# Kernel tuning notes

Measured on AMD Instinct MI355X. Metric: run time of the kernel, lower is better.

## Reference

```python
import jax, jax.numpy as jnp
import numpy as np

EMBED_DIM = 1024
NUM_HEADS = 16
D_K = EMBED_DIM // NUM_HEADS
SEQ = 4096
BATCH = 1


def setup_inputs() -> dict:
    key = jax.random.key(0)
    ks = jax.random.split(key, 9)
    s = 1.0 / np.sqrt(EMBED_DIM)
    return {
        "x": jax.random.normal(ks[0], (BATCH, SEQ, EMBED_DIM), dtype=jnp.float32),
        "Wq": jax.random.normal(ks[1], (EMBED_DIM, EMBED_DIM), dtype=jnp.float32) * s,
        "bq": jax.random.normal(ks[2], (EMBED_DIM,), dtype=jnp.float32) * 0.02,
        "Wk": jax.random.normal(ks[3], (EMBED_DIM, EMBED_DIM), dtype=jnp.float32) * s,
        "bk": jax.random.normal(ks[4], (EMBED_DIM,), dtype=jnp.float32) * 0.02,
        "Wv": jax.random.normal(ks[5], (EMBED_DIM, EMBED_DIM), dtype=jnp.float32) * s,
        "bv": jax.random.normal(ks[6], (EMBED_DIM,), dtype=jnp.float32) * 0.02,
        "Wo": jax.random.normal(ks[7], (EMBED_DIM, EMBED_DIM), dtype=jnp.float32) * s,
        "bo": jax.random.normal(ks[8], (EMBED_DIM,), dtype=jnp.float32) * 0.02,
    }


def reference(x, Wq, bq, Wk, bk, Wv, bv, Wo, bo):
    B, S, E = x.shape
    H, Dk = NUM_HEADS, D_K

    def split_heads(t):  # [B,S,E] -> [B,H,S,Dk]
        return t.reshape(B, S, H, Dk).transpose(0, 2, 1, 3)

    Q = split_heads(x @ Wq.T + bq)
    K = split_heads(x @ Wk.T + bk)
    V = split_heads(x @ Wv.T + bv)

    scores = jnp.einsum("bhqd,bhkd->bhqk", Q, K) / jnp.sqrt(jnp.float32(Dk))
    causal = jnp.tril(jnp.ones((S, S), dtype=bool))
    scores = jnp.where(causal, scores, -jnp.inf)
    attn = jax.nn.softmax(scores, axis=-1)
    out = jnp.einsum("bhqk,bhkd->bhqd", attn, V)  # [B,H,S,Dk]
    out = out.transpose(0, 2, 1, 3).reshape(B, S, E)
    return out @ Wo.T + bo
```

## Files before the change

kernel.cpp:

```cpp
#include <hip/hip_runtime.h>
#include <hip/hip_bf16.h>
#include <math.h>

#define SEQ 4096
#define EMB 1024
#define NH  16
#define DK  64

typedef __attribute__((ext_vector_type(8))) unsigned short us8;
typedef __attribute__((ext_vector_type(8))) short         s8;
typedef __attribute__((ext_vector_type(4))) unsigned short us4;
typedef __attribute__((ext_vector_type(4))) float          f4;

static __device__ __forceinline__ unsigned short f2bf(float f) {
    union { float f; unsigned u; } v; v.f = f;
    unsigned r = v.u + 0x7FFF + ((v.u >> 16) & 1);
    return (unsigned short)(r >> 16);
}

__device__ __forceinline__ void gl2lds16(const void* g, void* l) {
    __builtin_amdgcn_global_load_lds((const __attribute__((address_space(1))) void*)g,
                                     (__attribute__((address_space(3))) void*)l, 16, 0, 0);
}

__device__ __forceinline__ int pkbf(float a, float b) {
    return (int)__builtin_amdgcn_perm(__float_as_uint(a), __float_as_uint(b), 0x07060302u);
}

__global__ void cvt_all(const float* __restrict__ x,
                        const float* __restrict__ w0, const float* __restrict__ w1,
                        const float* __restrict__ w2, const float* __restrict__ w3,
                        unsigned short* __restrict__ xo,
                        unsigned short* __restrict__ o0, unsigned short* __restrict__ o1,
                        unsigned short* __restrict__ o2, unsigned short* __restrict__ o3) {
    const int idx = blockIdx.x * 256 + threadIdx.x;
    const float* in;
    unsigned short* out;
    int off;
    if (idx < (1 << 20)) { in = x; out = xo; off = idx; }
    else {
        const int t = idx - (1 << 20);
        const int w = t >> 18;
        off = t & ((1 << 18) - 1);
        in  = w == 0 ? w0 : (w == 1 ? w1 : (w == 2 ? w2 : w3));
        out = w == 0 ? o0 : (w == 1 ? o1 : (w == 2 ? o2 : o3));
    }
    const float4 v = ((const float4*)in)[off];
    us4 o;
    o[0] = f2bf(v.x); o[1] = f2bf(v.y); o[2] = f2bf(v.z); o[3] = f2bf(v.w);
    ((us4*)out)[off] = o;
}

__global__ __launch_bounds__(256) void transpose_kernel(
    const unsigned short* __restrict__ in, unsigned short* __restrict__ out) {
    __shared__ unsigned short t[64][72];
    const int tid = threadIdx.x;
    const int row = tid >> 2, c = (tid & 3) * 16;
    const int gr = blockIdx.x * 64, gc = blockIdx.y * 64;
    const unsigned short* src = in + (size_t)(gr + row) * EMB + gc + c;
    *(us8*)&t[row][c]     = *(const us8*)src;
    *(us8*)&t[row][c + 8] = *(const us8*)(src + 8);
    __syncthreads();
    us8 o0, o1;
#pragma unroll
    for (int j = 0; j < 8; ++j) { o0[j] = t[c + j][row]; o1[j] = t[c + 8 + j][row]; }
    const int a_   = c >> 4;
    const int base = (a_ >> 1) * 32 + (a_ & 1) * 4;
    us4 g0, g1, g2, g3;
#pragma unroll
    for (int i = 0; i < 4; ++i) { g0[i] = o0[i]; g1[i] = o0[4 + i]; g2[i] = o1[i]; g3[i] = o1[4 + i]; }
    unsigned short* dst = out + (size_t)(gc + row) * SEQ + gr + base;
    *(us4*)dst        = g0;
    *(us4*)(dst + 8)  = g1;
    *(us4*)(dst + 16) = g2;
    *(us4*)(dst + 24) = g3;
}

__global__ __launch_bounds__(256) void qkv_gemm(
    const unsigned short* __restrict__ X,
    const unsigned short* __restrict__ Wq, const unsigned short* __restrict__ Wk,
    const unsigned short* __restrict__ Wv,
    const float* __restrict__ bq, const float* __restrict__ bk, const float* __restrict__ bv,
    unsigned short* __restrict__ Qo, unsigned short* __restrict__ Ko, unsigned short* __restrict__ Vo)
{
    __shared__ unsigned short As[128 * 64];
    __shared__ unsigned short Bs[128 * 64];

    const int region = blockIdx.y >> 3;
    const unsigned short* W   = region == 0 ? Wq : (region == 1 ? Wk : Wv);
    const float*         bias = region == 0 ? bq : (region == 1 ? bk : bv);
    unsigned short*      out  = region == 0 ? Qo : (region == 1 ? Ko : Vo);
    const float scale = region == 0 ? 0.18033688011112042f : 1.0f;

    const int tid  = threadIdx.x;
    const int wave = tid >> 6;
    const int lane = tid & 63;
    const int quad = lane >> 4;
    const int l16  = lane & 15;
    const int wm   = (wave >> 1) * 64;
    const int wn   = (wave & 1) * 64;
    const int bm   = blockIdx.x * 128;
    const int bn   = (blockIdx.y & 7) * 128;

    f4 acc[4][4];
#pragma unroll
    for (int a = 0; a < 4; ++a)
#pragma unroll
        for (int b = 0; b < 4; ++b) acc[a][b] = (f4){0, 0, 0, 0};

    const int rsub = lane >> 3;
    const int gc   = ((lane & 7) ^ rsub) * 8;
    const int swz  = l16 & 7;

    for (int k0 = 0; k0 < EMB; k0 += 64) {
        __syncthreads();
#pragma unroll
        for (int i = 0; i < 4; ++i) {
            const int cb = i * 4 + wave;
            const int r  = cb * 8 + rsub;
            gl2lds16(X + (size_t)(bm + r) * EMB + k0 + gc, &As[cb * 512]);
            gl2lds16(W + (size_t)(bn + r) * EMB + k0 + gc, &Bs[cb * 512]);
        }
        __syncthreads();
#pragma unroll
        for (int kc = 0; kc < 2; ++kc) {
            s8 af[4], bf[4];
#pragma unroll
            for (int t = 0; t < 4; ++t) {
                const int seg = (kc * 4 + quad) ^ swz;
                af[t] = *(const s8*)&As[(wm + t * 16 + l16) * 64 + seg * 8];
                bf[t] = *(const s8*)&Bs[(wn + t * 16 + l16) * 64 + seg * 8];
            }
#pragma unroll
            for (int tm = 0; tm < 4; ++tm)
#pragma unroll
                for (int tn = 0; tn < 4; ++tn)
                    acc[tm][tn] = __builtin_amdgcn_mfma_f32_16x16x32_bf16(af[tm], bf[tn], acc[tm][tn], 0, 0, 0);
        }
    }

#pragma unroll
    for (int tn = 0; tn < 4; ++tn) {
        const int n = bn + wn + tn * 16 + l16;
        const float bv2 = bias[n];
#pragma unroll
        for (int tm = 0; tm < 4; ++tm)
#pragma unroll
            for (int rr = 0; rr < 4; ++rr) {
                const int m = bm + wm + tm * 16 + quad * 4 + rr;
                out[(size_t)m * EMB + n] = f2bf((acc[tm][tn][rr] + bv2) * scale);
            }
    }
}

__global__ __launch_bounds__(256) void gemm_op(
    const unsigned short* __restrict__ A, const unsigned short* __restrict__ B,
    const float* __restrict__ bias, float* __restrict__ C)
{
    __shared__ unsigned short As[128 * 64];
    __shared__ unsigned short Bs[64 * 64];

    const int tid  = threadIdx.x;
    const int wave = tid >> 6;
    const int lane = tid & 63;
    const int quad = lane >> 4;
    const int l16  = lane & 15;
    const int wm   = (wave >> 1) * 64;
    const int wn   = (wave & 1) * 32;
    const int bm   = blockIdx.x * 128;
    const int bn   = blockIdx.y * 64;

    f4 acc[4][2];
#pragma unroll
    for (int a = 0; a < 4; ++a) { acc[a][0] = (f4){0,0,0,0}; acc[a][1] = (f4){0,0,0,0}; }

    const int rsub = lane >> 3;
    const int gc   = ((lane & 7) ^ rsub) * 8;
    const int swz  = l16 & 7;

    for (int k0 = 0; k0 < EMB; k0 += 64) {
        __syncthreads();
#pragma unroll
        for (int i = 0; i < 6; ++i) {
            const int cb = i * 4 + wave;
            if (cb < 16) {
                gl2lds16(A + (size_t)(bm + cb * 8 + rsub) * EMB + k0 + gc, &As[cb * 512]);
            } else {
                const int c2 = cb - 16;
                gl2lds16(B + (size_t)(bn + c2 * 8 + rsub) * EMB + k0 + gc, &Bs[c2 * 512]);
            }
        }
        __syncthreads();
#pragma unroll
        for (int kc = 0; kc < 2; ++kc) {
            const int seg = (kc * 4 + quad) ^ swz;
            s8 af[4], bf[2];
#pragma unroll
            for (int t = 0; t < 4; ++t)
                af[t] = *(const s8*)&As[(wm + t * 16 + l16) * 64 + seg * 8];
#pragma unroll
            for (int t = 0; t < 2; ++t)
                bf[t] = *(const s8*)&Bs[(wn + t * 16 + l16) * 64 + seg * 8];
#pragma unroll
            for (int tm = 0; tm < 4; ++tm)
#pragma unroll
                for (int tn = 0; tn < 2; ++tn)
                    acc[tm][tn] = __builtin_amdgcn_mfma_f32_16x16x32_bf16(af[tm], bf[tn], acc[tm][tn], 0, 0, 0);
        }
    }

#pragma unroll
    for (int tn = 0; tn < 2; ++tn) {
        const int n = bn + wn + tn * 16 + l16;
        const float bv2 = bias[n];
#pragma unroll
        for (int tm = 0; tm < 4; ++tm)
#pragma unroll
            for (int rr = 0; rr < 4; ++rr) {
                const int m = bm + wm + tm * 16 + quad * 4 + rr;
                C[(size_t)m * EMB + n] = acc[tm][tn][rr] + bv2;
            }
    }
}

__global__ __launch_bounds__(512) void attn_kernel(
    const unsigned short* __restrict__ Qg, const unsigned short* __restrict__ Kg,
    const unsigned short* __restrict__ Vtg, unsigned short* __restrict__ Og)
{
    __shared__ unsigned short Ks[2][64][72];
    __shared__ unsigned short Vs[2][64][72];

    const int tid  = threadIdx.x;
    const int wave = tid >> 6;
    const int lane = tid & 63;
    const int quad = lane >> 4;
    const int l16  = lane & 15;
    const int h    = blockIdx.x;
    const int y    = blockIdx.y;
    const int u    = (y < 16) ? y : 47 - y;
    const int jmax = 63 - u;
    const int tileMine = (wave < 4) ? (63 - u) : u;
    const int jmine    = (wave < 4) ? jmax : u;
    const int colbase = h * DK;
    const int wrow0 = tileMine * 64 + (wave & 3) * 16;
    const int q_own = wrow0 + l16;

    s8 qf[2];
    {
        const unsigned short* q = Qg + (size_t)q_own * EMB + colbase + quad * 8;
        qf[0] = *(const s8*)(q);
        qf[1] = *(const s8*)(q + 32);
    }

    const int row = tid >> 3;
    const int c0  = (tid & 7) * 8;
    const unsigned short* kptr = Kg  + (size_t)row * EMB + colbase + c0;
    const unsigned short* vptr = Vtg + (size_t)(colbase + row) * SEQ + c0;

    us8 kr = *(const us8*)kptr;
    us8 vr = *(const us8*)vptr;
    *(us8*)&Ks[0][row][c0] = kr;
    *(us8*)&Vs[0][row][c0] = vr;
    kr = *(const us8*)(kptr + (size_t)64 * EMB);
    vr = *(const us8*)(vptr + 64);

    float l_i = 0.0f;
    f4 o[4];
#pragma unroll
    for (int t = 0; t < 4; ++t) o[t] = (f4){0, 0, 0, 0};

    for (int j = 0; j <= jmax; ++j) {
        __syncthreads();
        const int cur = j & 1;
        if (j < jmax) {
            const int nxt = cur ^ 1;
            *(us8*)&Ks[nxt][row][c0] = kr;
            *(us8*)&Vs[nxt][row][c0] = vr;
            if (j + 1 < jmax) {
                kr = *(const us8*)(kptr + (size_t)(j + 2) * 64 * EMB);
                vr = *(const us8*)(vptr + (j + 2) * 64);
            }
        }

        if (j <= jmine) {
            f4 s[4] = { {0,0,0,0}, {0,0,0,0}, {0,0,0,0}, {0,0,0,0} };
#pragma unroll
            for (int kc = 0; kc < 2; ++kc)
#pragma unroll
                for (int t = 0; t < 4; ++t) {
                    s8 kv = *(const s8*)&Ks[cur][t * 16 + l16][kc * 32 + quad * 8];
                    s[t] = __builtin_amdgcn_mfma_f32_16x16x32_bf16(kv, qf[kc], s[t], 0, 0, 0);
                }

            if (j == jmine) {
#pragma unroll
                for (int t = 0; t < 4; ++t) {
                    const int kb = j * 64 + t * 16 + quad * 4;
#pragma unroll
                    for (int r = 0; r < 4; ++r)
                        if (kb + r > q_own) s[t][r] = -1e30f;
                }
            }

            float rs = 0.0f;
#pragma unroll
            for (int t = 0; t < 4; ++t)
#pragma unroll
                for (int r = 0; r < 4; ++r) {
                    const float p = __builtin_amdgcn_exp2f(s[t][r]);
                    s[t][r] = p;
                    rs += p;
                }
            rs += __shfl_xor(rs, 16);
            rs += __shfl_xor(rs, 32);
            l_i += rs;

            union { int i[8]; s8 v[2]; } pku;
#pragma unroll
            for (int t = 0; t < 4; ++t) {
                pku.i[t * 2]     = pkbf(s[t][1], s[t][0]);
                pku.i[t * 2 + 1] = pkbf(s[t][3], s[t][2]);
            }

#pragma unroll
            for (int kc = 0; kc < 2; ++kc)
#pragma unroll
                for (int t = 0; t < 4; ++t) {
                    s8 va = *(const s8*)&Vs[cur][t * 16 + l16][kc * 32 + quad * 8];
                    o[t] = __builtin_amdgcn_mfma_f32_16x16x32_bf16(va, pku.v[kc], o[t], 0, 0, 0);
                }
        }
    }

    const float inv = 1.0f / l_i;
#pragma unroll
    for (int t = 0; t < 4; ++t) {
        us4 ov;
#pragma unroll
        for (int r = 0; r < 4; ++r) ov[r] = f2bf(o[t][r] * inv);
        *(us4*)&Og[(size_t)q_own * EMB + colbase + t * 16 + quad * 4] = ov;
    }
}

extern "C" void kernel_launch(void* const* d_in, const int* in_sizes, int n_in,
                              void* d_out, int out_size, void* d_ws, size_t ws_size,
                              hipStream_t stream) {
    const float* x  = (const float*)d_in[0];
    const float* Wq = (const float*)d_in[1];
    const float* bq = (const float*)d_in[2];
    const float* Wk = (const float*)d_in[3];
    const float* bk = (const float*)d_in[4];
    const float* Wv = (const float*)d_in[5];
    const float* bv = (const float*)d_in[6];
    const float* Wo = (const float*)d_in[7];
    const float* bo = (const float*)d_in[8];
    float* out = (float*)d_out;

    unsigned short* ws = (unsigned short*)d_ws;
    unsigned short* xb  = ws;
    unsigned short* Wqb = xb  + (size_t)SEQ * EMB;
    unsigned short* Wkb = Wqb + (size_t)EMB * EMB;
    unsigned short* Wvb = Wkb + (size_t)EMB * EMB;
    unsigned short* Wob = Wvb + (size_t)EMB * EMB;
    unsigned short* Qb  = Wob + (size_t)EMB * EMB;
    unsigned short* Kb  = Qb  + (size_t)SEQ * EMB;
    unsigned short* Vtb = Kb  + (size_t)SEQ * EMB;
    unsigned short* Ab  = Vtb + (size_t)SEQ * EMB;

    cvt_all<<<8192, 256, 0, stream>>>(x, Wq, Wk, Wv, Wo, xb, Wqb, Wkb, Wvb, Wob);

    qkv_gemm<<<dim3(SEQ / 128, 24), 256, 0, stream>>>(xb, Wqb, Wkb, Wvb, bq, bk, bv, Qb, Kb, Ab);

    transpose_kernel<<<dim3(SEQ / 64, EMB / 64), 256, 0, stream>>>(Ab, Vtb);

    attn_kernel<<<dim3(NH, 32), 512, 0, stream>>>(Qb, Kb, Vtb, Ab);

    gemm_op<<<dim3(SEQ / 128, EMB / 64), 256, 0, stream>>>(Ab, Wob, bo, out);
}
```

Baseline: 209.6 us.

## Process two 16-row query groups per wave in attention to reuse K/V fragments

The attention block is cut from 8 waves to 4, and each wave now handles 32 query rows as two 16-row groups. Each K and V fragment read from LDS feeds two MFMAs instead of one, which halves LDS read traffic per unit of compute. Each thread also loads twice as much K/V per tile. The cost is more registers per wave and fewer waves per block to hide latency, since the grid size is unchanged.

Result: slower. 227.3 us (+8.5%).

```diff
diff --git a/kernel.cpp b/kernel.cpp
--- a/kernel.cpp
+++ b/kernel.cpp
@@ -223,7 +223,7 @@
     }
 }
 
-__global__ __launch_bounds__(512) void attn_kernel(
+__global__ __launch_bounds__(256) void attn_kernel(
     const unsigned short* __restrict__ Qg, const unsigned short* __restrict__ Kg,
     const unsigned short* __restrict__ Vtg, unsigned short* __restrict__ Og)
 {
@@ -239,57 +239,73 @@
     const int y    = blockIdx.y;
     const int u    = (y < 16) ? y : 47 - y;
     const int jmax = 63 - u;
-    const int tileMine = (wave < 4) ? (63 - u) : u;
-    const int jmine    = (wave < 4) ? jmax : u;
+    const int tileMine = (wave < 2) ? (63 - u) : u;
+    const int jmine    = (wave < 2) ? jmax : u;
     const int colbase = h * DK;
-    const int wrow0 = tileMine * 64 + (wave & 3) * 16;
+    const int wrow0 = tileMine * 64 + (wave & 1) * 32;
     const int q_own = wrow0 + l16;
 
-    s8 qf[2];
-    {
-        const unsigned short* q = Qg + (size_t)q_own * EMB + colbase + quad * 8;
-        qf[0] = *(const s8*)(q);
-        qf[1] = *(const s8*)(q + 32);
-    }
-
-    const int row = tid >> 3;
-    const int c0  = (tid & 7) * 8;
+    s8 qf[2][2];
+#pragma unroll
+    for (int g2 = 0; g2 < 2; ++g2) {
+        const unsigned short* q = Qg + (size_t)(q_own + 16 * g2) * EMB + colbase + quad * 8;
+        qf[g2][0] = *(const s8*)(q);
+        qf[g2][1] = *(const s8*)(q + 32);
+    }
+
+    const int row = tid >> 2;
+    const int c0  = (tid & 3) * 16;
     const unsigned short* kptr = Kg  + (size_t)row * EMB + colbase + c0;
     const unsigned short* vptr = Vtg + (size_t)(colbase + row) * SEQ + c0;
 
-    us8 kr = *(const us8*)kptr;
-    us8 vr = *(const us8*)vptr;
-    *(us8*)&Ks[0][row][c0] = kr;
-    *(us8*)&Vs[0][row][c0] = vr;
-    kr = *(const us8*)(kptr + (size_t)64 * EMB);
-    vr = *(const us8*)(vptr + 64);
-
-    float l_i = 0.0f;
-    f4 o[4];
-#pragma unroll
-    for (int t = 0; t < 4; ++t) o[t] = (f4){0, 0, 0, 0};
+    us8 kr0 = *(const us8*)kptr, kr1 = *(const us8*)(kptr + 8);
+    us8 vr0 = *(const us8*)vptr, vr1 = *(const us8*)(vptr + 8);
+    *(us8*)&Ks[0][row][c0]     = kr0;
+    *(us8*)&Ks[0][row][c0 + 8] = kr1;
+    *(us8*)&Vs[0][row][c0]     = vr0;
+    *(us8*)&Vs[0][row][c0 + 8] = vr1;
+    kr0 = *(const us8*)(kptr + (size_t)64 * EMB);
+    kr1 = *(const us8*)(kptr + (size_t)64 * EMB + 8);
+    vr0 = *(const us8*)(vptr + 64);
+    vr1 = *(const us8*)(vptr + 64 + 8);
+
+    float l_i[2] = {0.0f, 0.0f};
+    f4 o[2][4];
+#pragma unroll
+    for (int g2 = 0; g2 < 2; ++g2)
+#pragma unroll
+        for (int t = 0; t < 4; ++t) o[g2][t] = (f4){0, 0, 0, 0};
 
     for (int j = 0; j <= jmax; ++j) {
         __syncthreads();
         const int cur = j & 1;
         if (j < jmax) {
             const int nxt = cur ^ 1;
-            *(us8*)&Ks[nxt][row][c0] = kr;
-            *(us8*)&Vs[nxt][row][c0] = vr;
+            *(us8*)&Ks[nxt][row][c0]     = kr0;
+            *(us8*)&Ks[nxt][row][c0 + 8] = kr1;
+            *(us8*)&Vs[nxt][row][c0]     = vr0;
+            *(us8*)&Vs[nxt][row][c0 + 8] = vr1;
             if (j + 1 < jmax) {
-                kr = *(const us8*)(kptr + (size_t)(j + 2) * 64 * EMB);
-                vr = *(const us8*)(vptr + (j + 2) * 64);
+                const unsigned short* kn = kptr + (size_t)(j + 2) * 64 * EMB;
+                const unsigned short* vn = vptr + (j + 2) * 64;
+                kr0 = *(const us8*)kn;  kr1 = *(const us8*)(kn + 8);
+                vr0 = *(const us8*)vn;  vr1 = *(const us8*)(vn + 8);
             }
         }
 
         if (j <= jmine) {
-            f4 s[4] = { {0,0,0,0}, {0,0,0,0}, {0,0,0,0}, {0,0,0,0} };
+            f4 s[2][4];
+#pragma unroll
+            for (int g2 = 0; g2 < 2; ++g2)
+#pragma unroll
+                for (int t = 0; t < 4; ++t) s[g2][t] = (f4){0, 0, 0, 0};
 #pragma unroll
             for (int kc = 0; kc < 2; ++kc)
 #pragma unroll
                 for (int t = 0; t < 4; ++t) {
                     s8 kv = *(const s8*)&Ks[cur][t * 16 + l16][kc * 32 + quad * 8];
-                    s[t] = __builtin_amdgcn_mfma_f32_16x16x32_bf16(kv, qf[kc], s[t], 0, 0, 0);
+                    s[0][t] = __builtin_amdgcn_mfma_f32_16x16x32_bf16(kv, qf[0][kc], s[0][t], 0, 0, 0);
+                    s[1][t] = __builtin_amdgcn_mfma_f32_16x16x32_bf16(kv, qf[1][kc], s[1][t], 0, 0, 0);
                 }
 
             if (j == jmine) {
@@ -297,29 +313,33 @@
                 for (int t = 0; t < 4; ++t) {
                     const int kb = j * 64 + t * 16 + quad * 4;
 #pragma unroll
-                    for (int r = 0; r < 4; ++r)
-                        if (kb + r > q_own) s[t][r] = -1e30f;
+                    for (int r = 0; r < 4; ++r) {
+                        if (kb + r > q_own)      s[0][t][r] = -1e30f;
+                        if (kb + r > q_own + 16) s[1][t][r] = -1e30f;
+                    }
                 }
             }
 
-            float rs = 0.0f;
-#pragma unroll
-            for (int t = 0; t < 4; ++t)
-#pragma unroll
-                for (int r = 0; r < 4; ++r) {
-                    const float p = __builtin_amdgcn_exp2f(s[t][r]);
-                    s[t][r] = p;
-                    rs += p;
+            union { int i[8]; s8 v[2]; } pku[2];
+#pragma unroll
+            for (int g2 = 0; g2 < 2; ++g2) {
+                float rs = 0.0f;
+#pragma unroll
+                for (int t = 0; t < 4; ++t)
+#pragma unroll
+                    for (int r = 0; r < 4; ++r) {
+                        const float p = __builtin_amdgcn_exp2f(s[g2][t][r]);
+                        s[g2][t][r] = p;
+                        rs += p;
+                    }
+                rs += __shfl_xor(rs, 16);
+                rs += __shfl_xor(rs, 32);
+                l_i[g2] += rs;
+#pragma unroll
+                for (int t = 0; t < 4; ++t) {
+                    pku[g2].i[t * 2]     = pkbf(s[g2][t][1], s[g2][t][0]);
+                    pku[g2].i[t * 2 + 1] = pkbf(s[g2][t][3], s[g2][t][2]);
                 }
-            rs += __shfl_xor(rs, 16);
-            rs += __shfl_xor(rs, 32);
-            l_i += rs;
-
-            union { int i[8]; s8 v[2]; } pku;
-#pragma unroll
-            for (int t = 0; t < 4; ++t) {
-                pku.i[t * 2]     = pkbf(s[t][1], s[t][0]);
-                pku.i[t * 2 + 1] = pkbf(s[t][3], s[t][2]);
             }
 
 #pragma unroll
@@ -327,18 +347,22 @@
 #pragma unroll
                 for (int t = 0; t < 4; ++t) {
                     s8 va = *(const s8*)&Vs[cur][t * 16 + l16][kc * 32 + quad * 8];
-                    o[t] = __builtin_amdgcn_mfma_f32_16x16x32_bf16(va, pku.v[kc], o[t], 0, 0, 0);
+                    o[0][t] = __builtin_amdgcn_mfma_f32_16x16x32_bf16(va, pku[0].v[kc], o[0][t], 0, 0, 0);
+                    o[1][t] = __builtin_amdgcn_mfma_f32_16x16x32_bf16(va, pku[1].v[kc], o[1][t], 0, 0, 0);
                 }
         }
     }
 
-    const float inv = 1.0f / l_i;
-#pragma unroll
-    for (int t = 0; t < 4; ++t) {
-        us4 ov;
-#pragma unroll
-        for (int r = 0; r < 4; ++r) ov[r] = f2bf(o[t][r] * inv);
-        *(us4*)&Og[(size_t)q_own * EMB + colbase + t * 16 + quad * 4] = ov;
+#pragma unroll
+    for (int g2 = 0; g2 < 2; ++g2) {
+        const float inv = 1.0f / l_i[g2];
+#pragma unroll
+        for (int t = 0; t < 4; ++t) {
+            us4 ov;
+#pragma unroll
+            for (int r = 0; r < 4; ++r) ov[r] = f2bf(o[g2][t][r] * inv);
+            *(us4*)&Og[(size_t)(q_own + 16 * g2) * EMB + colbase + t * 16 + quad * 4] = ov;
+        }
     }
 }
 
@@ -373,7 +397,7 @@
 
     transpose_kernel<<<dim3(SEQ / 64, EMB / 64), 256, 0, stream>>>(Ab, Vtb);
 
-    attn_kernel<<<dim3(NH, 32), 512, 0, stream>>>(Qb, Kb, Vtb, Ab);
+    attn_kernel<<<dim3(NH, 32), 256, 0, stream>>>(Qb, Kb, Vtb, Ab);
 
     gemm_op<<<dim3(SEQ / 128, EMB / 64), 256, 0, stream>>>(Ab, Wob, bo, out);
 }
```
